# Kernel optimization log

Measured on AMD Instinct MI355X. Metric: run time of the kernel, lower is better.

Reference implementation:

```python
import jax, jax.numpy as jnp
import numpy as np

B, S, D, DK, DV = 8, 2048, 256, 128, 128

def setup_inputs() -> dict:
    key = jax.random.key(0)
    ks = jax.random.split(key, 9)
    return {
        "x_q": jax.random.normal(ks[0], (B, S, D), jnp.float32),
        "x_k": jax.random.normal(ks[1], (B, S, D), jnp.float32),
        "x_v": jax.random.normal(ks[2], (B, S, D), jnp.float32),
        "Wq": jax.random.normal(ks[3], (D, DK), jnp.float32) * (1.0 / np.sqrt(D)),
        "bq": jax.random.normal(ks[4], (DK,), jnp.float32) * 0.02,
        "Wk": jax.random.normal(ks[5], (D, DK), jnp.float32) * (1.0 / np.sqrt(D)),
        "bk": jax.random.normal(ks[6], (DK,), jnp.float32) * 0.02,
        "Wv": jax.random.normal(ks[7], (D, DV), jnp.float32) * (1.0 / np.sqrt(D)),
        "bv": jax.random.normal(ks[8], (DV,), jnp.float32) * 0.02,
    }

def reference(x_q, x_k, x_v, Wq, bq, Wk, bk, Wv, bv):
    # Dense projections: [B,S,D] @ [D,dk] + bias
    q = jnp.einsum("bsd,dk->bsk", x_q, Wq) + bq
    k = jnp.einsum("bsd,dk->bsk", x_k, Wk) + bk
    v = jnp.einsum("bsd,dv->bsv", x_v, Wv) + bv
    scale = 1.0 / np.sqrt(Wq.shape[1]).astype(np.float32)  # 1/sqrt(d_k)
    scores = jnp.einsum("bqk,bsk->bqs", q, k) * scale       # [B,S,S]
    attn = jax.nn.softmax(scores, axis=-1)
    return jnp.einsum("bqs,bsv->bqv", attn, v)               # [B,S,d_v]
```

## Files before the change

kernel.cpp:

```cpp
#include <hip/hip_runtime.h>
#include <stdint.h>

typedef float    f32x4  __attribute__((ext_vector_type(4)));
typedef float    f32x16 __attribute__((ext_vector_type(16)));
typedef _Float16 f16x8  __attribute__((ext_vector_type(8)));
typedef _Float16 f16x4  __attribute__((ext_vector_type(4)));

#define SPLIT 4
#define NTILES 16

__device__ __forceinline__ f32x4 mfma16(f16x8 a, f16x8 b, f32x4 c) {
    return __builtin_amdgcn_mfma_f32_16x16x32_f16(a, b, c, 0, 0, 0);
}
__device__ __forceinline__ f32x16 mfma32(f16x8 a, f16x8 b, f32x16 c) {
    return __builtin_amdgcn_mfma_f32_32x32x16_f16(a, b, c, 0, 0, 0);
}
__device__ __forceinline__ void gll16(const _Float16* g, _Float16* l) {
    __builtin_amdgcn_global_load_lds(
        (const __attribute__((address_space(1))) void*)g,
        (__attribute__((address_space(3))) void*)l, 16, 0, 0);
}
__device__ __forceinline__ void drain_vm() {
    __builtin_amdgcn_sched_barrier(0);
    asm volatile("s_waitcnt vmcnt(0)" ::: "memory");
    __builtin_amdgcn_sched_barrier(0);
}

__global__ __launch_bounds__(256) void prep_weights(
    const float* __restrict__ Wq, const float* __restrict__ Wk,
    const float* __restrict__ Wv, _Float16* __restrict__ wt) {
    __shared__ float Ls[64 * 65];
    const int bx = blockIdx.x;
    const int w  = bx >> 3, t = bx & 7;
    const int k0 = (t >> 1) * 64, n0 = (t & 1) * 64;
    const float* W = (w == 0) ? Wq : (w == 1) ? Wk : Wv;
    const int tid = threadIdx.x;
    #pragma unroll
    for (int i = 0; i < 16; i++) {
        int idx = i * 256 + tid;
        int r = idx >> 6, c = idx & 63;
        Ls[r * 65 + c] = W[(k0 + r) * 128 + n0 + c];
    }
    __syncthreads();
    #pragma unroll
    for (int i = 0; i < 16; i++) {
        int idx = i * 256 + tid;
        int r2 = idx >> 6, c2 = idx & 63;
        wt[w * 32768 + (n0 + r2) * 256 + k0 + c2] = (_Float16)Ls[c2 * 65 + r2];
    }
}

__global__ __launch_bounds__(256) void proj_kernel(
    const float* __restrict__ xq, const float* __restrict__ xk,
    const float* __restrict__ xv, const _Float16* __restrict__ wt,
    const float* __restrict__ bq, const float* __restrict__ bk,
    const float* __restrict__ bv,
    _Float16* __restrict__ qo, _Float16* __restrict__ ko,
    _Float16* __restrict__ vt)
{
    const int mode = blockIdx.y;
    const float*    X    = mode == 0 ? xq : mode == 1 ? xk : xv;
    const float*    bias = mode == 0 ? bq : mode == 1 ? bk : bv;
    const _Float16* W    = wt + mode * 32768;

    __shared__ __align__(16) _Float16 Ls[128 * 66];

    const int tid  = threadIdx.x;
    const int wave = tid >> 6, lane = tid & 63;
    const int ln   = lane & 15, qd = lane >> 4;
    const int row0 = blockIdx.x * 64 + wave * 16;

    const float*    xrow = X + (size_t)(row0 + ln) * 256 + qd * 8;
    const _Float16* wb   = W + ln * 256 + qd * 8;

    f32x4 acc[8];
    #pragma unroll
    for (int i = 0; i < 8; i++) acc[i] = (f32x4){0.f, 0.f, 0.f, 0.f};

    #pragma unroll
    for (int kk = 0; kk < 8; kk++) {
        f32x4 a0 = *(const f32x4*)(xrow + kk * 32);
        f32x4 a1 = *(const f32x4*)(xrow + kk * 32 + 4);
        f16x8 af;
        af[0] = (_Float16)a0[0]; af[1] = (_Float16)a0[1];
        af[2] = (_Float16)a0[2]; af[3] = (_Float16)a0[3];
        af[4] = (_Float16)a1[0]; af[5] = (_Float16)a1[1];
        af[6] = (_Float16)a1[2]; af[7] = (_Float16)a1[3];
        #pragma unroll
        for (int nt = 0; nt < 8; nt++) {
            f16x8 bf = *(const f16x8*)(wb + nt * 4096 + kk * 32);
            acc[nt] = mfma16(af, bf, acc[nt]);
        }
    }

    const float SC = 0.08838834764831845f * 1.4426950408889634f;
    if (mode != 2) {
        _Float16* Y = mode == 0 ? qo : ko;
        #pragma unroll
        for (int nt = 0; nt < 8; nt++) {
            int col = nt * 16 + ln;
            float bb = bias[col];
            #pragma unroll
            for (int r = 0; r < 4; r++) {
                int orow = row0 + qd * 4 + r;
                float val = acc[nt][r] + bb;
                if (mode == 0) val *= SC;
                Y[(size_t)orow * 128 + col] = (_Float16)val;
            }
        }
    } else {
        #pragma unroll
        for (int nt = 0; nt < 8; nt++) {
            int col = nt * 16 + ln;
            float bb = bias[col];
            #pragma unroll
            for (int r = 0; r < 4; r++) {
                int srow = wave * 16 + qd * 4 + r;
                Ls[col * 66 + srow] = (_Float16)(acc[nt][r] + bb);
            }
        }
        __syncthreads();
        const int bb2 = row0 >> 11;
        const int s0  = (blockIdx.x * 64) & 2047;
        #pragma unroll
        for (int i = 0; i < 4; i++) {
            int g  = i * 256 + tid;
            int dv = g >> 3, off = (g & 7) * 8;
            f16x8 v8 = *(const f16x8*)&Ls[dv * 66 + off];
            *(f16x8*)(vt + ((size_t)(bb2 * 128 + dv)) * 2048 + s0 + off) = v8;
        }
    }
}

__global__ __launch_bounds__(256, 3) void attn_kernel(
    const _Float16* __restrict__ qp, const _Float16* __restrict__ kp,
    const _Float16* __restrict__ vtp, _Float16* __restrict__ opart,
    float2* __restrict__ ml)
{
    const int bid = blockIdx.x;
    const int gx  = bid & 7;
    const int q0i = (bid >> 3) & 15;
    const int gg  = bid >> 7;
    const int g   = gg * 8 + gx;
    const int b   = g >> 2;
    const int z   = g & 3;
    const int q0  = q0i * 128;

    const int tid  = threadIdx.x;
    const int wave = tid >> 6, lane = tid & 63;
    const int ln   = lane & 31, h = lane >> 5;

    __shared__ __align__(16) _Float16 smem[16896];

    int koff[8], voff[2][4];
    #pragma unroll
    for (int kb = 0; kb < 8; kb++)
        koff[kb] = ln * 128 + (((kb * 2 + h) ^ (ln & 15)) * 8);
    const int vsw = (ln >> 1) & 3;
    #pragma unroll
    for (int kb2 = 0; kb2 < 2; kb2++)
        #pragma unroll
        for (int dvb = 0; dvb < 4; dvb++)
            voff[kb2][dvb] =
                8192 + (dvb * 32 + ln) * 32 + (((kb2 * 2 + h) ^ vsw) * 8);
    int kidx[2], vidx[2], dst[2];
    #pragma unroll
    for (int j = 0; j < 2; j++) {
        int p = wave * 128 + j * 64 + lane;
        int r = p >> 4, c = p & 15;
        kidx[j] = r * 128 + ((c ^ (r & 15)) * 8);
        vidx[j] = (p >> 2) * 2048 + (((p & 3) ^ ((p >> 3) & 3)) * 8);
        dst[j]  = (wave * 128 + j * 64) * 8;
    }

    const _Float16* qbase =
        qp + (size_t)(b * 2048 + q0 + wave * 32 + ln) * 128 + h * 8;
    f16x8 qf[8];
    #pragma unroll
    for (int kb = 0; kb < 8; kb++) qf[kb] = *(const f16x8*)(qbase + kb * 16);

    f32x16 o[4];
    #pragma unroll
    for (int i = 0; i < 4; i++) o[i] = (f32x16){};
    float m_run = -1e30f, l_run = 0.f;

    const _Float16* kbase = kp + (size_t)b * 2048 * 128;
    const _Float16* vbase = vtp + (size_t)b * 128 * 2048;
    const int kt0 = z * NTILES;

    auto stage = [&](int kt, int buf) {
        const _Float16* ks = kbase + (size_t)kt * 4096;
        const _Float16* vs = vbase + kt * 32;
        _Float16* kdst = smem + buf * 4096;
        _Float16* vdst = smem + 8192 + buf * 4096;
        #pragma unroll
        for (int j = 0; j < 2; j++) {
            gll16(ks + kidx[j], kdst + dst[j]);
            gll16(vs + vidx[j], vdst + dst[j]);
        }
    };

    auto do_tile = [&](const int BUF) {
        const int KO = BUF * 4096, VO = BUF * 4096;
        f32x16 sc = (f32x16){};
        __builtin_amdgcn_s_setprio(1);
        #pragma unroll
        for (int kb = 0; kb < 8; kb++) {
            f16x8 kf = *(const f16x8*)&smem[KO + koff[kb]];
            sc = mfma32(kf, qf[kb], sc);
        }
        __builtin_amdgcn_s_setprio(0);
        float t = sc[0];
        #pragma unroll
        for (int i = 1; i < 16; i++) t = fmaxf(t, sc[i]);
        t = fmaxf(t, __shfl_xor(t, 32));
        const float mnew  = fmaxf(m_run, t);
        const float alpha = exp2f(m_run - mnew);

        f16x4 phg[4];
        float ssum = 0.f;
        #pragma unroll
        for (int gi = 0; gi < 4; gi++) {
            #pragma unroll
            for (int e = 0; e < 4; e++) {
                float p = exp2f(sc[gi * 4 + e] - mnew);
                ssum += p;
                phg[gi][e] = (_Float16)p;
            }
        }
        ssum += __shfl_xor(ssum, 32);
        l_run = l_run * alpha + ssum;
        m_run = mnew;

        if (__any(alpha < 1.0f)) {
            #pragma unroll
            for (int dvb = 0; dvb < 4; dvb++) o[dvb] *= alpha;
        }

        #pragma unroll
        for (int kb2 = 0; kb2 < 2; kb2++) {
            f16x4 own0 = phg[2 * kb2], own1 = phg[2 * kb2 + 1];
            f16x4 send = h ? own0 : own1;
            unsigned long long sv = __builtin_bit_cast(unsigned long long, send);
            unsigned long long rv = __shfl_xor(sv, 32);
            f16x4 recv = __builtin_bit_cast(f16x4, rv);
            f16x4 lo = h ? recv : own0;
            f16x4 hi = h ? own1 : recv;
            f16x8 bf = __builtin_shufflevector(lo, hi, 0, 1, 2, 3, 4, 5, 6, 7);
            __builtin_amdgcn_s_setprio(1);
            #pragma unroll
            for (int dvb = 0; dvb < 4; dvb++) {
                f16x8 vf = *(const f16x8*)&smem[VO + voff[kb2][dvb]];
                o[dvb] = mfma32(vf, bf, o[dvb]);
            }
            __builtin_amdgcn_s_setprio(0);
        }
    };

    stage(kt0, 0);
    #pragma unroll 1
    for (int ht = 0; ht < NTILES / 2; ht++) {
        drain_vm();
        __syncthreads();
        if (2 * ht + 1 < NTILES) stage(kt0 + 2 * ht + 1, 1);
        do_tile(0);
        drain_vm();
        __syncthreads();
        if (2 * ht + 2 < NTILES) stage(kt0 + 2 * ht + 2, 0);
        do_tile(1);
    }

    drain_vm();
    __syncthreads();
    _Float16* pw = smem + wave * 4224;
    #pragma unroll
    for (int dvb = 0; dvb < 4; dvb++) {
        #pragma unroll
        for (int gi = 0; gi < 4; gi++) {
            f16x4 w4;
            #pragma unroll
            for (int e = 0; e < 4; e++) w4[e] = (_Float16)o[dvb][gi * 4 + e];
            *(f16x4*)&pw[ln * 132 + dvb * 32 + gi * 8 + h * 4] = w4;
        }
    }
    const size_t prow = (size_t)(z * 8 + b) * 2048 + q0 + wave * 32;
    __builtin_amdgcn_s_waitcnt(0);
    #pragma unroll
    for (int p = 0; p < 2; p++) {
        int q = p * 16 + (lane >> 2), part = lane & 3;
        #pragma unroll
        for (int i2 = 0; i2 < 4; i2++) {
            f16x8 v8 = *(const f16x8*)&pw[q * 132 + part * 8 + i2 * 32];
            *(f16x8*)(opart + (prow + q) * 128 + part * 8 + i2 * 32) = v8;
        }
    }
    if (lane < 32) {
        float2 v; v.x = m_run; v.y = l_run;
        ml[prow + ln] = v;
    }
}

__global__ __launch_bounds__(256) void merge_kernel(
    const _Float16* __restrict__ opart, const float2* __restrict__ ml,
    float* __restrict__ out)
{
    const int t = threadIdx.x;
    const int r = t >> 4, cg = t & 15;
    const size_t row = (size_t)blockIdx.x * 16 + r;

    float M = -1e30f;
    #pragma unroll
    for (int zi = 0; zi < SPLIT; zi++)
        M = fmaxf(M, ml[(size_t)zi * 16384 + row].x);
    float L = 0.f;
    float acc[8] = {0.f, 0.f, 0.f, 0.f, 0.f, 0.f, 0.f, 0.f};
    #pragma unroll
    for (int zi = 0; zi < SPLIT; zi++) {
        float2 p = ml[(size_t)zi * 16384 + row];
        float w = exp2f(p.x - M);
        L += w * p.y;
        f16x8 v = *(const f16x8*)&opart[((size_t)zi * 16384 + row) * 128 + cg * 8];
        #pragma unroll
        for (int j = 0; j < 8; j++) acc[j] += w * (float)v[j];
    }
    const float inv = 1.0f / L;
    float* op = out + row * 128 + cg * 8;
    f32x4 lo = (f32x4){acc[0] * inv, acc[1] * inv, acc[2] * inv, acc[3] * inv};
    f32x4 hi = (f32x4){acc[4] * inv, acc[5] * inv, acc[6] * inv, acc[7] * inv};
    *(f32x4*)op = lo;
    *(f32x4*)(op + 4) = hi;
}

extern "C" void kernel_launch(void* const* d_in, const int* in_sizes, int n_in,
                              void* d_out, int out_size, void* d_ws, size_t ws_size,
                              hipStream_t stream) {
    const float* xq = (const float*)d_in[0];
    const float* xk = (const float*)d_in[1];
    const float* xv = (const float*)d_in[2];
    const float* Wq = (const float*)d_in[3];
    const float* bq = (const float*)d_in[4];
    const float* Wk = (const float*)d_in[5];
    const float* bk = (const float*)d_in[6];
    const float* Wv = (const float*)d_in[7];
    const float* bv = (const float*)d_in[8];
    float* out = (float*)d_out;

    char* ws = (char*)d_ws;
    _Float16* wt    = (_Float16*)ws;
    _Float16* qo    = (_Float16*)(ws + 196608);
    _Float16* ko    = (_Float16*)(ws + 196608 + 4194304);
    _Float16* vt    = (_Float16*)(ws + 196608 + 2 * 4194304);
    float2*   ml    = (float2*)  (ws + 196608 + 3 * 4194304);
    _Float16* opart = (_Float16*)(ws + 196608 + 3 * 4194304 + 1048576);

    hipLaunchKernelGGL(prep_weights, dim3(24), dim3(256), 0, stream,
                       Wq, Wk, Wv, wt);
    hipLaunchKernelGGL(proj_kernel, dim3(256, 3), dim3(256), 0, stream,
                       xq, xk, xv, wt, bq, bk, bv, qo, ko, vt);
    hipLaunchKernelGGL(attn_kernel, dim3(16 * 8 * SPLIT), dim3(256), 0, stream,
                       qo, ko, vt, opart, ml);
    hipLaunchKernelGGL(merge_kernel, dim3(1024), dim3(256), 0, stream,
                       opart, ml, out);
}
```

Measured before the change: 161.6 us.

## Use 512-thread attention blocks covering 256 query rows sharing K/V tiles

The attention kernel now launches 8-wave blocks that each own 256 query rows, and the grid shrinks from 512 to 256 blocks. Each staged K/V tile in LDS is reused by twice as many waves, which halves the global-to-LDS traffic per query. The block-to-(batch, split, query) mapping changes, and each thread now issues one async load per tile instead of two. In exchange there are fewer resident blocks, a larger LDS footprint per block and wider barrier synchronisation.

```diff
diff --git a/kernel.cpp b/kernel.cpp
--- a/kernel.cpp
+++ b/kernel.cpp
@@ -132,25 +132,23 @@
     }
 }
 
-__global__ __launch_bounds__(256, 3) void attn_kernel(
+__global__ __launch_bounds__(512, 2) void attn_kernel(
     const _Float16* __restrict__ qp, const _Float16* __restrict__ kp,
     const _Float16* __restrict__ vtp, _Float16* __restrict__ opart,
     float2* __restrict__ ml)
 {
     const int bid = blockIdx.x;
     const int gx  = bid & 7;
-    const int q0i = (bid >> 3) & 15;
-    const int gg  = bid >> 7;
-    const int g   = gg * 8 + gx;
-    const int b   = g >> 2;
-    const int z   = g & 3;
-    const int q0  = q0i * 128;
+    const int q0i = (bid >> 3) & 7;
+    const int z   = bid >> 6;
+    const int b   = gx;
+    const int q0  = q0i * 256;
 
     const int tid  = threadIdx.x;
     const int wave = tid >> 6, lane = tid & 63;
     const int ln   = lane & 31, h = lane >> 5;
 
-    __shared__ __align__(16) _Float16 smem[16896];
+    __shared__ __align__(16) _Float16 smem[33792];
 
     int koff[8], voff[2][4];
     #pragma unroll
@@ -163,15 +161,10 @@
         for (int dvb = 0; dvb < 4; dvb++)
             voff[kb2][dvb] =
                 8192 + (dvb * 32 + ln) * 32 + (((kb2 * 2 + h) ^ vsw) * 8);
-    int kidx[2], vidx[2], dst[2];
-    #pragma unroll
-    for (int j = 0; j < 2; j++) {
-        int p = wave * 128 + j * 64 + lane;
-        int r = p >> 4, c = p & 15;
-        kidx[j] = r * 128 + ((c ^ (r & 15)) * 8);
-        vidx[j] = (p >> 2) * 2048 + (((p & 3) ^ ((p >> 3) & 3)) * 8);
-        dst[j]  = (wave * 128 + j * 64) * 8;
-    }
+    const int p    = wave * 64 + lane;
+    const int kidx = (p >> 4) * 128 + (((p & 15) ^ ((p >> 4) & 15)) * 8);
+    const int vidx = (p >> 2) * 2048 + (((p & 3) ^ ((p >> 3) & 3)) * 8);
+    const int dst  = wave * 512;
 
     const _Float16* qbase =
         qp + (size_t)(b * 2048 + q0 + wave * 32 + ln) * 128 + h * 8;
@@ -191,13 +184,8 @@
     auto stage = [&](int kt, int buf) {
         const _Float16* ks = kbase + (size_t)kt * 4096;
         const _Float16* vs = vbase + kt * 32;
-        _Float16* kdst = smem + buf * 4096;
-        _Float16* vdst = smem + 8192 + buf * 4096;
-        #pragma unroll
-        for (int j = 0; j < 2; j++) {
-            gll16(ks + kidx[j], kdst + dst[j]);
-            gll16(vs + vidx[j], vdst + dst[j]);
-        }
+        gll16(ks + kidx, smem + buf * 4096 + dst);
+        gll16(vs + vidx, smem + 8192 + buf * 4096 + dst);
     };
 
     auto do_tile = [&](const int BUF) {
@@ -223,9 +211,9 @@
         for (int gi = 0; gi < 4; gi++) {
             #pragma unroll
             for (int e = 0; e < 4; e++) {
-                float p = exp2f(sc[gi * 4 + e] - mnew);
-                ssum += p;
-                phg[gi][e] = (_Float16)p;
+                float p2 = exp2f(sc[gi * 4 + e] - mnew);
+                ssum += p2;
+                phg[gi][e] = (_Float16)p2;
             }
         }
         ssum += __shfl_xor(ssum, 32);
@@ -286,8 +274,8 @@
     const size_t prow = (size_t)(z * 8 + b) * 2048 + q0 + wave * 32;
     __builtin_amdgcn_s_waitcnt(0);
     #pragma unroll
-    for (int p = 0; p < 2; p++) {
-        int q = p * 16 + (lane >> 2), part = lane & 3;
+    for (int pp = 0; pp < 2; pp++) {
+        int q = pp * 16 + (lane >> 2), part = lane & 3;
         #pragma unroll
         for (int i2 = 0; i2 < 4; i2++) {
             f16x8 v8 = *(const f16x8*)&pw[q * 132 + part * 8 + i2 * 32];
@@ -357,7 +345,7 @@
                        Wq, Wk, Wv, wt);
     hipLaunchKernelGGL(proj_kernel, dim3(256, 3), dim3(256), 0, stream,
                        xq, xk, xv, wt, bq, bk, bv, qo, ko, vt);
-    hipLaunchKernelGGL(attn_kernel, dim3(16 * 8 * SPLIT), dim3(256), 0, stream,
+    hipLaunchKernelGGL(attn_kernel, dim3(8 * 8 * SPLIT), dim3(512), 0, stream,
                        qo, ko, vt, opart, ml);
     hipLaunchKernelGGL(merge_kernel, dim3(1024), dim3(256), 0, stream,
                        opart, ml, out);
```

Result: no change. 159.1 us (-1.5%).
